# Performance work log

Hardware: AMD Instinct MI355X
Metric: run time of the kernel (lower is better)

The kernel has to match this reference:

```python
import jax, jax.numpy as jnp
import numpy as np

H = 5  # hidden size of both LSTMs

def _lstm_layer(x, Wih, Whh, bih, bhh):
    """x: [B,T,I] -> hs: [B,T,H]. PyTorch gate order i,f,g,o; zero init state."""
    B, T, _ = x.shape
    # precompute input contribution for all timesteps: [T,B,4H]
    xg = (jnp.einsum('bti,gi->btg', x, Wih) + bih + bhh).transpose(1, 0, 2)
    def step(carry, xg_t):
        h, c = carry
        g = xg_t + h @ Whh.T
        i, f, gg, o = jnp.split(g, 4, axis=-1)
        c = jax.nn.sigmoid(f) * c + jax.nn.sigmoid(i) * jnp.tanh(gg)
        h = jax.nn.sigmoid(o) * jnp.tanh(c)
        return (h, c), h
    h0 = jnp.zeros((B, H), x.dtype)
    (_, _), hs = jax.lax.scan(step, (h0, h0), xg)
    return hs.transpose(1, 0, 2)  # [B,T,H]

def setup_inputs() -> dict:
    key = jax.random.key(0)
    ks = jax.random.split(key, 32)
    B, T = 16384, 128
    def u(k, shape, fan):
        s = 1.0 / np.sqrt(fan)
        return jax.random.uniform(k, shape, jnp.float32, -s, s)
    inp = {
        'x1': jax.random.normal(ks[0], (B, T, 5), jnp.float32),
        'x2': jax.random.normal(ks[1], (B, T, 5), jnp.float32),
        # lstm1 (1 layer)
        'Wih1': u(ks[2], (4*H, 5), H), 'Whh1': u(ks[3], (4*H, H), H),
        'bih1': u(ks[4], (4*H,), H), 'bhh1': u(ks[5], (4*H,), H),
        # lstm2 layer 0
        'Wih2a': u(ks[6], (4*H, 5), H), 'Whh2a': u(ks[7], (4*H, H), H),
        'bih2a': u(ks[8], (4*H,), H), 'bhh2a': u(ks[9], (4*H,), H),
        # lstm2 layer 1
        'Wih2b': u(ks[10], (4*H, H), H), 'Whh2b': u(ks[11], (4*H, H), H),
        'bih2b': u(ks[12], (4*H,), H), 'bhh2b': u(ks[13], (4*H,), H),
        # FC stack 20->32->32->16->16->5
        'W1': u(ks[14], (32, 20), 20), 'b1': u(ks[15], (32,), 20),
        'W2': u(ks[16], (32, 32), 32), 'b2': u(ks[17], (32,), 32),
        'W3': u(ks[18], (16, 32), 32), 'b3': u(ks[19], (16,), 32),
        'W4': u(ks[20], (16, 16), 16), 'b4': u(ks[21], (16,), 16),
        'W5': u(ks[22], (5, 16), 16), 'b5': u(ks[23], (5,), 16),
    }
    return inp

def reference(x1, x2, Wih1, Whh1, bih1, bhh1, Wih2a, Whh2a, bih2a, bhh2a,
              Wih2b, Whh2b, bih2b, bhh2b, W1, b1, W2, b2, W3, b3, W4, b4, W5, b5):
    out1 = _lstm_layer(x1, Wih1, Whh1, bih1, bhh1)[:, -1, :]            # [B,5]
    h2 = _lstm_layer(x2, Wih2a, Whh2a, bih2a, bhh2a)                    # [B,T,5]
    out2 = _lstm_layer(h2, Wih2b, Whh2b, bih2b, bhh2b)[:, -1, :]        # [B,5]
    out = jnp.concatenate([x1[:, -1, :], x2[:, -1, :], out1, out2], axis=1)  # [B,20]
    out = jax.nn.relu(out @ W1.T + b1)
    out = jax.nn.relu(out @ W2.T + b2)
    out = jax.nn.relu(out @ W3.T + b3)
    out = jax.nn.relu(out @ W4.T + b4)
    return out @ W5.T + b5  # [B,5]
```

## Files before the change

kernel.cpp:

```cpp
#include <hip/hip_runtime.h>

#define DEV __device__ __forceinline__
#define KSIG (-1.442695041f)
#define KTANH (-2.885390082f)

typedef float f2 __attribute__((ext_vector_type(2)));

DEV float fexp2(float x) { return __builtin_amdgcn_exp2f(x); }
DEV float frcp(float x) { return __builtin_amdgcn_rcpf(x); }
DEV float bperm(int a, float x) {
  return __int_as_float(__builtin_amdgcn_ds_bpermute(a, __float_as_int(x)));
}
DEV f2 pkfma(f2 a, f2 b, f2 c) { return __builtin_elementwise_fma(a, b, c); }

struct CellP {
  f2 wx[4][2];
  f2 wh[4][2];
  float wx4[4], wh4[4];
  f2 b2[4];
};

DEV void load_cellP(CellP& W, int u, const float* __restrict__ Wih,
                    const float* __restrict__ Whh,
                    const float* __restrict__ bih,
                    const float* __restrict__ bhh) {
#pragma unroll
  for (int rt = 0; rt < 4; ++rt) {
    int row = 5 * rt + u;
    float kx = (rt == 2) ? KTANH : KSIG;
    W.wx[rt][0] = (f2){kx * Wih[row * 5 + 0], kx * Wih[row * 5 + 1]};
    W.wx[rt][1] = (f2){kx * Wih[row * 5 + 2], kx * Wih[row * 5 + 3]};
    W.wx4[rt] = kx * Wih[row * 5 + 4];
    W.wh[rt][0] = (f2){kx * Whh[row * 5 + 0], kx * Whh[row * 5 + 1]};
    W.wh[rt][1] = (f2){kx * Whh[row * 5 + 2], kx * Whh[row * 5 + 3]};
    W.wh4[rt] = kx * Whh[row * 5 + 4];
    W.b2[rt] = (f2){kx * (bih[row] + bhh[row]), 0.f};
  }
}

DEV float stepP(const CellP& W, const f2 xp[2], float x4, float hAll[5],
                float& c, const int bp[5]) {
  f2 hp0 = (f2){hAll[0], hAll[1]};
  f2 hp1 = (f2){hAll[2], hAll[3]};
  float acc[4];
#pragma unroll
  for (int rt = 0; rt < 4; ++rt) {
    f2 a2 = pkfma(W.wx[rt][0], xp[0], W.b2[rt]);
    a2 = pkfma(W.wx[rt][1], xp[1], a2);
    a2 = pkfma(W.wh[rt][0], hp0, a2);
    a2 = pkfma(W.wh[rt][1], hp1, a2);
    float a = a2.x + a2.y;
    a = fmaf(W.wx4[rt], x4, a);
    acc[rt] = fmaf(W.wh4[rt], hAll[4], a);
  }
  float gi = frcp(1.f + fexp2(acc[0]));
  float gf = frcp(1.f + fexp2(acc[1]));
  float gg = fmaf(2.f, frcp(1.f + fexp2(acc[2])), -1.f);
  float go = frcp(1.f + fexp2(acc[3]));
  c = fmaf(gf, c, gi * gg);
  float th = fmaf(2.f, frcp(1.f + fexp2(KTANH * c)), -1.f);
  float h = go * th;
#pragma unroll
  for (int u2 = 0; u2 < 5; ++u2) hAll[u2] = bperm(bp[u2], h);
  return h;
}

__global__ __launch_bounds__(192, 4) void rnn3w_kernel(
    const float* __restrict__ x1, const float* __restrict__ x2,
    const float* __restrict__ Wih1, const float* __restrict__ Whh1,
    const float* __restrict__ bih1, const float* __restrict__ bhh1,
    const float* __restrict__ Wih2a, const float* __restrict__ Whh2a,
    const float* __restrict__ bih2a, const float* __restrict__ bhh2a,
    const float* __restrict__ Wih2b, const float* __restrict__ Whh2b,
    const float* __restrict__ bih2b, const float* __restrict__ bhh2b,
    const float* __restrict__ W1, const float* __restrict__ b1,
    const float* __restrict__ W2, const float* __restrict__ b2,
    const float* __restrict__ W3, const float* __restrict__ b3,
    const float* __restrict__ W4, const float* __restrict__ b4,
    const float* __restrict__ W5, const float* __restrict__ b5,
    float* __restrict__ out, int B) {
  __shared__ float sH[2][64];
  __shared__ float sIn[12][20];
  __shared__ float sA[12][32];
  __shared__ float sB[12][32];

  const int tid = threadIdx.x;
  const int w = tid >> 6;
  const int l = tid & 63;
  const int g = l / 5;
  const int u = l - 5 * g;
  const bool act = (g < 12);
  const int el = act ? g : 11;
  const int eg = blockIdx.x * 12 + el;
  const int egc = (eg < B) ? eg : (B - 1);

  CellP W;
  if (w == 0)
    load_cellP(W, u, Wih1, Whh1, bih1, bhh1);
  else if (w == 1)
    load_cellP(W, u, Wih2a, Whh2a, bih2a, bhh2a);
  else
    load_cellP(W, u, Wih2b, Whh2b, bih2b, bhh2b);

  int bp[5];
#pragma unroll
  for (int u2 = 0; u2 < 5; ++u2) bp[u2] = (5 * g + u2) * 4;

  const float* px = ((w == 0) ? x1 : x2) + (size_t)egc * 640;

  if (tid < 128) sH[tid >> 6][tid & 63] = 0.f;

  float hAll[5];
  float c = 0.f, hOwn = 0.f;
#pragma unroll
  for (int k = 0; k < 5; ++k) hAll[k] = 0.f;

  f2 xp[2];
  float x4 = 0.f;
  if (w < 2) {
    xp[0] = (f2){px[0], px[1]};
    xp[1] = (f2){px[2], px[3]};
    x4 = px[4];
  }
  __syncthreads();

  for (int t = 0; t < 128; ++t) {
    f2 xin[2];
    float xin4;
    if (w == 2) {
      const float* s = &sH[(t + 1) & 1][g * 5];
      xin[0] = (f2){s[0], s[1]};
      xin[1] = (f2){s[2], s[3]};
      xin4 = s[4];
    } else {
      xin[0] = xp[0];
      xin[1] = xp[1];
      xin4 = x4;
    }
    if (w < 2) {
      const int tn = (t < 127) ? t + 1 : 127;
      xp[0] = (f2){px[tn * 5 + 0], px[tn * 5 + 1]};
      xp[1] = (f2){px[tn * 5 + 2], px[tn * 5 + 3]};
      x4 = px[tn * 5 + 4];
    }
    hOwn = stepP(W, xin, xin4, hAll, c, bp);
    if (w == 2 && t == 0) {
#pragma unroll
      for (int k = 0; k < 5; ++k) hAll[k] = 0.f;
      c = 0.f;
      hOwn = 0.f;
    }
    if (w == 1 && act) sH[t & 1][g * 5 + u] = hOwn;
    __syncthreads();
  }

  if (w == 2) {
    const float* s = &sH[1][g * 5];
    f2 xin[2] = {(f2){s[0], s[1]}, (f2){s[2], s[3]}};
    hOwn = stepP(W, xin, s[4], hAll, c, bp);
  }

  if (act) {
    if (w == 0) {
      sIn[el][u] = x1[(size_t)egc * 640 + 635 + u];
      sIn[el][10 + u] = hOwn;
    } else if (w == 1) {
      sIn[el][5 + u] = x2[(size_t)egc * 640 + 635 + u];
    } else {
      sIn[el][15 + u] = hOwn;
    }
  }
  __syncthreads();

  for (int task = tid; task < 12 * 32; task += 192) {
    int e = task >> 5, n = task & 31;
    float acc = b1[n];
#pragma unroll
    for (int k = 0; k < 20; ++k) acc = fmaf(W1[n * 20 + k], sIn[e][k], acc);
    sA[e][n] = fmaxf(acc, 0.f);
  }
  __syncthreads();
  for (int task = tid; task < 12 * 32; task += 192) {
    int e = task >> 5, n = task & 31;
    float acc = b2[n];
#pragma unroll
    for (int k = 0; k < 32; ++k) acc = fmaf(W2[n * 32 + k], sA[e][k], acc);
    sB[e][n] = fmaxf(acc, 0.f);
  }
  __syncthreads();
  {
    int e = tid >> 4, n = tid & 15;
    float acc = b3[n];
#pragma unroll
    for (int k = 0; k < 32; ++k) acc = fmaf(W3[n * 32 + k], sB[e][k], acc);
    sA[e][n] = fmaxf(acc, 0.f);
  }
  __syncthreads();
  {
    int e = tid >> 4, n = tid & 15;
    float acc = b4[n];
#pragma unroll
    for (int k = 0; k < 16; ++k) acc = fmaf(W4[n * 16 + k], sA[e][k], acc);
    sB[e][n] = fmaxf(acc, 0.f);
  }
  __syncthreads();
  if (tid < 60) {
    int e = tid / 5, n = tid - 5 * (tid / 5);
    float acc = b5[n];
#pragma unroll
    for (int k = 0; k < 16; ++k) acc = fmaf(W5[n * 16 + k], sB[e][k], acc);
    int ego = blockIdx.x * 12 + e;
    if (ego < B) out[(size_t)ego * 5 + n] = acc;
  }
}

extern "C" void kernel_launch(void* const* d_in, const int* in_sizes, int n_in,
                              void* d_out, int out_size, void* d_ws,
                              size_t ws_size, hipStream_t stream) {
  const float* x1 = (const float*)d_in[0];
  const float* x2 = (const float*)d_in[1];
  const float* Wih1 = (const float*)d_in[2];
  const float* Whh1 = (const float*)d_in[3];
  const float* bih1 = (const float*)d_in[4];
  const float* bhh1 = (const float*)d_in[5];
  const float* Wih2a = (const float*)d_in[6];
  const float* Whh2a = (const float*)d_in[7];
  const float* bih2a = (const float*)d_in[8];
  const float* bhh2a = (const float*)d_in[9];
  const float* Wih2b = (const float*)d_in[10];
  const float* Whh2b = (const float*)d_in[11];
  const float* bih2b = (const float*)d_in[12];
  const float* bhh2b = (const float*)d_in[13];
  const float* W1 = (const float*)d_in[14];
  const float* b1 = (const float*)d_in[15];
  const float* W2 = (const float*)d_in[16];
  const float* b2 = (const float*)d_in[17];
  const float* W3 = (const float*)d_in[18];
  const float* b3 = (const float*)d_in[19];
  const float* W4 = (const float*)d_in[20];
  const float* b4 = (const float*)d_in[21];
  const float* W5 = (const float*)d_in[22];
  const float* b5 = (const float*)d_in[23];

  int B = in_sizes[0] / 640;
  int nB = (B + 11) / 12;

  rnn3w_kernel<<<nB, 192, 0, stream>>>(
      x1, x2, Wih1, Whh1, bih1, bhh1, Wih2a, Whh2a, bih2a, bhh2a, Wih2b, Whh2b,
      bih2b, bhh2b, W1, b1, W2, b2, W3, b3, W4, b4, W5, b5, (float*)d_out, B);
}
```

Before: 223.5 us.

## Remove per-timestep block barriers by fusing stacked LSTM layers per wave

Instead of splitting the three LSTM layers across three waves joined by shared memory and a __syncthreads every timestep, each wave now runs independent sequences with no barriers. Wave 0 interleaves two lstm1 sequences, and waves 1 and 2 each run lstm2 layer0 and layer1 back to back within a single thread. Each block now handles 24 batch elements, and the FC stack loops are widened to match. The aim is to remove barrier stalls and give each wave two independent dependency chains for ILP, at the cost of more registers (launch bounds lowered to 2) and half as many blocks.

```diff
diff --git a/kernel.cpp b/kernel.cpp
--- a/kernel.cpp
+++ b/kernel.cpp
@@ -45,13 +45,13 @@
   float acc[4];
 #pragma unroll
   for (int rt = 0; rt < 4; ++rt) {
-    f2 a2 = pkfma(W.wx[rt][0], xp[0], W.b2[rt]);
+    f2 a2 = pkfma(W.wh[rt][0], hp0, W.b2[rt]);
+    a2 = pkfma(W.wh[rt][1], hp1, a2);
+    a2 = pkfma(W.wx[rt][0], xp[0], a2);
     a2 = pkfma(W.wx[rt][1], xp[1], a2);
-    a2 = pkfma(W.wh[rt][0], hp0, a2);
-    a2 = pkfma(W.wh[rt][1], hp1, a2);
     float a = a2.x + a2.y;
-    a = fmaf(W.wx4[rt], x4, a);
-    acc[rt] = fmaf(W.wh4[rt], hAll[4], a);
+    a = fmaf(W.wh4[rt], hAll[4], a);
+    acc[rt] = fmaf(W.wx4[rt], x4, a);
   }
   float gi = frcp(1.f + fexp2(acc[0]));
   float gf = frcp(1.f + fexp2(acc[1]));
@@ -65,7 +65,7 @@
   return h;
 }
 
-__global__ __launch_bounds__(192, 4) void rnn3w_kernel(
+__global__ __launch_bounds__(192, 2) void rnn_nosync_kernel(
     const float* __restrict__ x1, const float* __restrict__ x2,
     const float* __restrict__ Wih1, const float* __restrict__ Whh1,
     const float* __restrict__ bih1, const float* __restrict__ bhh1,
@@ -79,100 +79,96 @@
     const float* __restrict__ W4, const float* __restrict__ b4,
     const float* __restrict__ W5, const float* __restrict__ b5,
     float* __restrict__ out, int B) {
-  __shared__ float sH[2][64];
-  __shared__ float sIn[12][20];
-  __shared__ float sA[12][32];
-  __shared__ float sB[12][32];
+  __shared__ float sIn[24][20];
+  __shared__ float sA[24][32];
+  __shared__ float sB[24][32];
 
   const int tid = threadIdx.x;
   const int w = tid >> 6;
   const int l = tid & 63;
-  const int g = l / 5;
+  int g = l / 5;
   const int u = l - 5 * g;
   const bool act = (g < 12);
-  const int el = act ? g : 11;
-  const int eg = blockIdx.x * 12 + el;
-  const int egc = (eg < B) ? eg : (B - 1);
-
-  CellP W;
-  if (w == 0)
+  if (!act) g = 11;
+  const int base = blockIdx.x * 24;
+
+  int bp[5];
+#pragma unroll
+  for (int k = 0; k < 5; ++k) bp[k] = (5 * g + k) * 4;
+
+  if (w == 0) {
+    CellP W;
     load_cellP(W, u, Wih1, Whh1, bih1, bhh1);
-  else if (w == 1)
-    load_cellP(W, u, Wih2a, Whh2a, bih2a, bhh2a);
-  else
-    load_cellP(W, u, Wih2b, Whh2b, bih2b, bhh2b);
-
-  int bp[5];
-#pragma unroll
-  for (int u2 = 0; u2 < 5; ++u2) bp[u2] = (5 * g + u2) * 4;
-
-  const float* px = ((w == 0) ? x1 : x2) + (size_t)egc * 640;
-
-  if (tid < 128) sH[tid >> 6][tid & 63] = 0.f;
-
-  float hAll[5];
-  float c = 0.f, hOwn = 0.f;
-#pragma unroll
-  for (int k = 0; k < 5; ++k) hAll[k] = 0.f;
-
-  f2 xp[2];
-  float x4 = 0.f;
-  if (w < 2) {
-    xp[0] = (f2){px[0], px[1]};
-    xp[1] = (f2){px[2], px[3]};
-    x4 = px[4];
-  }
-  __syncthreads();
-
-  for (int t = 0; t < 128; ++t) {
-    f2 xin[2];
-    float xin4;
-    if (w == 2) {
-      const float* s = &sH[(t + 1) & 1][g * 5];
-      xin[0] = (f2){s[0], s[1]};
-      xin[1] = (f2){s[2], s[3]};
-      xin4 = s[4];
-    } else {
-      xin[0] = xp[0];
-      xin[1] = xp[1];
-      xin4 = x4;
-    }
-    if (w < 2) {
+    const int e0 = base + 2 * g, e1 = e0 + 1;
+    const int e0c = (e0 < B) ? e0 : B - 1;
+    const int e1c = (e1 < B) ? e1 : B - 1;
+    const float* p0 = x1 + (size_t)e0c * 640;
+    const float* p1 = x1 + (size_t)e1c * 640;
+    float hA[5], hB[5];
+    float cA = 0.f, cB = 0.f, hoA = 0.f, hoB = 0.f;
+#pragma unroll
+    for (int k = 0; k < 5; ++k) {
+      hA[k] = 0.f;
+      hB[k] = 0.f;
+    }
+    f2 xa[2] = {(f2){p0[0], p0[1]}, (f2){p0[2], p0[3]}};
+    f2 xb[2] = {(f2){p1[0], p1[1]}, (f2){p1[2], p1[3]}};
+    float xa4 = p0[4], xb4 = p1[4];
+    for (int t = 0; t < 128; ++t) {
+      f2 xia[2] = {xa[0], xa[1]}, xib[2] = {xb[0], xb[1]};
+      float xia4 = xa4, xib4 = xb4;
+      const int tn = (t < 127) ? t + 1 : 127;
+      xa[0] = (f2){p0[tn * 5 + 0], p0[tn * 5 + 1]};
+      xa[1] = (f2){p0[tn * 5 + 2], p0[tn * 5 + 3]};
+      xa4 = p0[tn * 5 + 4];
+      xb[0] = (f2){p1[tn * 5 + 0], p1[tn * 5 + 1]};
+      xb[1] = (f2){p1[tn * 5 + 2], p1[tn * 5 + 3]};
+      xb4 = p1[tn * 5 + 4];
+      hoA = stepP(W, xia, xia4, hA, cA, bp);
+      hoB = stepP(W, xib, xib4, hB, cB, bp);
+    }
+    if (act) {
+      sIn[2 * g][u] = x1[(size_t)e0c * 640 + 635 + u];
+      sIn[2 * g][10 + u] = hoA;
+      sIn[2 * g + 1][u] = x1[(size_t)e1c * 640 + 635 + u];
+      sIn[2 * g + 1][10 + u] = hoB;
+    }
+  } else {
+    CellP Wa, Wb;
+    load_cellP(Wa, u, Wih2a, Whh2a, bih2a, bhh2a);
+    load_cellP(Wb, u, Wih2b, Whh2b, bih2b, bhh2b);
+    const int el = ((w == 1) ? 0 : 12) + g;
+    const int e = base + el;
+    const int ec = (e < B) ? e : B - 1;
+    const float* px = x2 + (size_t)ec * 640;
+    float hA[5], hB[5];
+    float cA = 0.f, cB = 0.f, hoB = 0.f;
+#pragma unroll
+    for (int k = 0; k < 5; ++k) {
+      hA[k] = 0.f;
+      hB[k] = 0.f;
+    }
+    f2 xp[2] = {(f2){px[0], px[1]}, (f2){px[2], px[3]}};
+    float x4 = px[4];
+    for (int t = 0; t < 128; ++t) {
+      f2 xin[2] = {xp[0], xp[1]};
+      float xin4 = x4;
       const int tn = (t < 127) ? t + 1 : 127;
       xp[0] = (f2){px[tn * 5 + 0], px[tn * 5 + 1]};
       xp[1] = (f2){px[tn * 5 + 2], px[tn * 5 + 3]};
       x4 = px[tn * 5 + 4];
-    }
-    hOwn = stepP(W, xin, xin4, hAll, c, bp);
-    if (w == 2 && t == 0) {
-#pragma unroll
-      for (int k = 0; k < 5; ++k) hAll[k] = 0.f;
-      c = 0.f;
-      hOwn = 0.f;
-    }
-    if (w == 1 && act) sH[t & 1][g * 5 + u] = hOwn;
-    __syncthreads();
-  }
-
-  if (w == 2) {
-    const float* s = &sH[1][g * 5];
-    f2 xin[2] = {(f2){s[0], s[1]}, (f2){s[2], s[3]}};
-    hOwn = stepP(W, xin, s[4], hAll, c, bp);
-  }
-
-  if (act) {
-    if (w == 0) {
-      sIn[el][u] = x1[(size_t)egc * 640 + 635 + u];
-      sIn[el][10 + u] = hOwn;
-    } else if (w == 1) {
-      sIn[el][5 + u] = x2[(size_t)egc * 640 + 635 + u];
-    } else {
-      sIn[el][15 + u] = hOwn;
-    }
-  }
-  __syncthreads();
-
-  for (int task = tid; task < 12 * 32; task += 192) {
+      (void)stepP(Wa, xin, xin4, hA, cA, bp);
+      f2 hin[2] = {(f2){hA[0], hA[1]}, (f2){hA[2], hA[3]}};
+      hoB = stepP(Wb, hin, hA[4], hB, cB, bp);
+    }
+    if (act) {
+      sIn[el][5 + u] = x2[(size_t)ec * 640 + 635 + u];
+      sIn[el][15 + u] = hoB;
+    }
+  }
+  __syncthreads();
+
+  for (int task = tid; task < 24 * 32; task += 192) {
     int e = task >> 5, n = task & 31;
     float acc = b1[n];
 #pragma unroll
@@ -180,7 +176,7 @@
     sA[e][n] = fmaxf(acc, 0.f);
   }
   __syncthreads();
-  for (int task = tid; task < 12 * 32; task += 192) {
+  for (int task = tid; task < 24 * 32; task += 192) {
     int e = task >> 5, n = task & 31;
     float acc = b2[n];
 #pragma unroll
@@ -188,28 +184,28 @@
     sB[e][n] = fmaxf(acc, 0.f);
   }
   __syncthreads();
-  {
-    int e = tid >> 4, n = tid & 15;
+  for (int task = tid; task < 24 * 16; task += 192) {
+    int e = task >> 4, n = task & 15;
     float acc = b3[n];
 #pragma unroll
     for (int k = 0; k < 32; ++k) acc = fmaf(W3[n * 32 + k], sB[e][k], acc);
     sA[e][n] = fmaxf(acc, 0.f);
   }
   __syncthreads();
-  {
-    int e = tid >> 4, n = tid & 15;
+  for (int task = tid; task < 24 * 16; task += 192) {
+    int e = task >> 4, n = task & 15;
     float acc = b4[n];
 #pragma unroll
     for (int k = 0; k < 16; ++k) acc = fmaf(W4[n * 16 + k], sA[e][k], acc);
     sB[e][n] = fmaxf(acc, 0.f);
   }
   __syncthreads();
-  if (tid < 60) {
+  if (tid < 120) {
     int e = tid / 5, n = tid - 5 * (tid / 5);
     float acc = b5[n];
 #pragma unroll
     for (int k = 0; k < 16; ++k) acc = fmaf(W5[n * 16 + k], sB[e][k], acc);
-    int ego = blockIdx.x * 12 + e;
+    int ego = base + e;
     if (ego < B) out[(size_t)ego * 5 + n] = acc;
   }
 }
@@ -243,9 +239,9 @@
   const float* b5 = (const float*)d_in[23];
 
   int B = in_sizes[0] / 640;
-  int nB = (B + 11) / 12;
-
-  rnn3w_kernel<<<nB, 192, 0, stream>>>(
+  int nB = (B + 23) / 24;
+
+  rnn_nosync_kernel<<<nB, 192, 0, stream>>>(
       x1, x2, Wih1, Whh1, bih1, bhh1, Wih2a, Whh2a, bih2a, bhh2a, Wih2b, Whh2b,
       bih2b, bhh2b, W1, b1, W2, b2, W3, b3, W4, b4, W5, b5, (float*)d_out, B);
 }
```

Result: slower. 239.0 us (+6.9%).

## Map one batch element per lane with full LSTM cell held in registers

Applied to the files above, without the earlier changes.

Replaces the five-lanes-per-element layout, which exchanged hidden state through ds_bpermute, with one element per lane. Each lane computes all 20 gates with packed FMAs over weights held in registers. Inputs are loaded as 80-byte float4 chunks, double-buffered, and the time loop is unrolled by chunk with a bare s_barrier sync. Blocks now cover 64 elements, so there are far fewer blocks. In exchange, register pressure rises sharply (about 100 weight registers, hence launch_bounds(192,1)), and each lane's input reads are strided by 2560 bytes across lanes, so loads no longer coalesce.

```diff
diff --git a/kernel.cpp b/kernel.cpp
--- a/kernel.cpp
+++ b/kernel.cpp
@@ -5,67 +5,141 @@
 #define KTANH (-2.885390082f)
 
 typedef float f2 __attribute__((ext_vector_type(2)));
+typedef float f4 __attribute__((ext_vector_type(4)));
 
 DEV float fexp2(float x) { return __builtin_amdgcn_exp2f(x); }
 DEV float frcp(float x) { return __builtin_amdgcn_rcpf(x); }
-DEV float bperm(int a, float x) {
-  return __int_as_float(__builtin_amdgcn_ds_bpermute(a, __float_as_int(x)));
-}
 DEV f2 pkfma(f2 a, f2 b, f2 c) { return __builtin_elementwise_fma(a, b, c); }
 
-struct CellP {
-  f2 wx[4][2];
-  f2 wh[4][2];
-  float wx4[4], wh4[4];
-  f2 b2[4];
+DEV void pin2(f2& v) {
+  float a = v.x, b = v.y;
+  asm volatile("" : "+v"(a), "+v"(b));
+  v = (f2){a, b};
+}
+
+DEV void sync_lds() {
+  asm volatile("s_waitcnt lgkmcnt(0)\ns_barrier" ::: "memory");
+}
+
+struct CellU {
+  f2 wx[2][5][5];
+  f2 wh[2][5][5];
+  f2 bb[2][5];
 };
 
-DEV void load_cellP(CellP& W, int u, const float* __restrict__ Wih,
+DEV void load_cellU(CellU& W, const float* __restrict__ Wih,
                     const float* __restrict__ Whh,
                     const float* __restrict__ bih,
                     const float* __restrict__ bhh) {
 #pragma unroll
-  for (int rt = 0; rt < 4; ++rt) {
-    int row = 5 * rt + u;
-    float kx = (rt == 2) ? KTANH : KSIG;
-    W.wx[rt][0] = (f2){kx * Wih[row * 5 + 0], kx * Wih[row * 5 + 1]};
-    W.wx[rt][1] = (f2){kx * Wih[row * 5 + 2], kx * Wih[row * 5 + 3]};
-    W.wx4[rt] = kx * Wih[row * 5 + 4];
-    W.wh[rt][0] = (f2){kx * Whh[row * 5 + 0], kx * Whh[row * 5 + 1]};
-    W.wh[rt][1] = (f2){kx * Whh[row * 5 + 2], kx * Whh[row * 5 + 3]};
-    W.wh4[rt] = kx * Whh[row * 5 + 4];
-    W.b2[rt] = (f2){kx * (bih[row] + bhh[row]), 0.f};
-  }
-}
-
-DEV float stepP(const CellP& W, const f2 xp[2], float x4, float hAll[5],
-                float& c, const int bp[5]) {
-  f2 hp0 = (f2){hAll[0], hAll[1]};
-  f2 hp1 = (f2){hAll[2], hAll[3]};
-  float acc[4];
-#pragma unroll
-  for (int rt = 0; rt < 4; ++rt) {
-    f2 a2 = pkfma(W.wx[rt][0], xp[0], W.b2[rt]);
-    a2 = pkfma(W.wx[rt][1], xp[1], a2);
-    a2 = pkfma(W.wh[rt][0], hp0, a2);
-    a2 = pkfma(W.wh[rt][1], hp1, a2);
-    float a = a2.x + a2.y;
-    a = fmaf(W.wx4[rt], x4, a);
-    acc[rt] = fmaf(W.wh4[rt], hAll[4], a);
-  }
-  float gi = frcp(1.f + fexp2(acc[0]));
-  float gf = frcp(1.f + fexp2(acc[1]));
-  float gg = fmaf(2.f, frcp(1.f + fexp2(acc[2])), -1.f);
-  float go = frcp(1.f + fexp2(acc[3]));
-  c = fmaf(gf, c, gi * gg);
-  float th = fmaf(2.f, frcp(1.f + fexp2(KTANH * c)), -1.f);
-  float h = go * th;
-#pragma unroll
-  for (int u2 = 0; u2 < 5; ++u2) hAll[u2] = bperm(bp[u2], h);
-  return h;
-}
-
-__global__ __launch_bounds__(192, 4) void rnn3w_kernel(
+  for (int j = 0; j < 5; ++j) {
+#pragma unroll
+    for (int k = 0; k < 5; ++k) {
+      W.wx[0][j][k] = (f2){KSIG * Wih[j * 5 + k], KSIG * Wih[(5 + j) * 5 + k]};
+      W.wx[1][j][k] =
+          (f2){KTANH * Wih[(10 + j) * 5 + k], KSIG * Wih[(15 + j) * 5 + k]};
+      W.wh[0][j][k] = (f2){KSIG * Whh[j * 5 + k], KSIG * Whh[(5 + j) * 5 + k]};
+      W.wh[1][j][k] =
+          (f2){KTANH * Whh[(10 + j) * 5 + k], KSIG * Whh[(15 + j) * 5 + k]};
+    }
+    W.bb[0][j] =
+        (f2){KSIG * (bih[j] + bhh[j]), KSIG * (bih[5 + j] + bhh[5 + j])};
+    W.bb[1][j] = (f2){KTANH * (bih[10 + j] + bhh[10 + j]),
+                      KSIG * (bih[15 + j] + bhh[15 + j])};
+  }
+}
+
+DEV void stepU(const CellU& W, float x0, float x1, float x2, float x3, float x4,
+               float h[5], float c[5]) {
+  f2 aIF[5], aGO[5];
+#pragma unroll
+  for (int j = 0; j < 5; ++j) {
+    aIF[j] = W.bb[0][j];
+    aGO[j] = W.bb[1][j];
+  }
+  float xs[5] = {x0, x1, x2, x3, x4};
+#pragma unroll
+  for (int k = 0; k < 5; ++k) {
+    f2 xk = (f2){xs[k], xs[k]};
+#pragma unroll
+    for (int j = 0; j < 5; ++j) {
+      aIF[j] = pkfma(W.wx[0][j][k], xk, aIF[j]);
+      aGO[j] = pkfma(W.wx[1][j][k], xk, aGO[j]);
+    }
+  }
+#pragma unroll
+  for (int k = 0; k < 5; ++k) {
+    f2 hk = (f2){h[k], h[k]};
+#pragma unroll
+    for (int j = 0; j < 5; ++j) {
+      aIF[j] = pkfma(W.wh[0][j][k], hk, aIF[j]);
+      aGO[j] = pkfma(W.wh[1][j][k], hk, aGO[j]);
+    }
+  }
+#pragma unroll
+  for (int j = 0; j < 5; ++j) {
+    float gi = frcp(1.f + fexp2(aIF[j].x));
+    float gf = frcp(1.f + fexp2(aIF[j].y));
+    float tg = fmaf(2.f, frcp(1.f + fexp2(aGO[j].x)), -1.f);
+    float go = frcp(1.f + fexp2(aGO[j].y));
+    c[j] = fmaf(gf, c[j], gi * tg);
+    float tc = fmaf(2.f, frcp(1.f + fexp2(KTANH * c[j])), -1.f);
+    h[j] = go * tc;
+  }
+}
+
+struct XBuf {
+  f4 a, b, c, d, e;
+};
+DEV void xload(XBuf& bf, const float* __restrict__ px, int ch) {
+  const f4* q = (const f4*)px + ch * 5;
+  bf.a = q[0];
+  bf.b = q[1];
+  bf.c = q[2];
+  bf.d = q[3];
+  bf.e = q[4];
+}
+
+#define STEP_S(S, RST, X0, X1, X2, X3, X4)                 \
+  {                                                        \
+    float xv0, xv1, xv2, xv3, xv4;                         \
+    if (w == 2) {                                          \
+      const int rb = ((S) + 1) & 1;                        \
+      xv0 = sH[rb][l][0];                                  \
+      xv1 = sH[rb][l][1];                                  \
+      xv2 = sH[rb][l][2];                                  \
+      xv3 = sH[rb][l][3];                                  \
+      xv4 = sH[rb][l][4];                                  \
+    } else {                                               \
+      xv0 = X0;                                            \
+      xv1 = X1;                                            \
+      xv2 = X2;                                            \
+      xv3 = X3;                                            \
+      xv4 = X4;                                            \
+    }                                                      \
+    stepU(W, xv0, xv1, xv2, xv3, xv4, h, c);               \
+    if (w == 1) {                                          \
+      const int wb = (S) & 1;                              \
+      sH[wb][l][0] = h[0];                                 \
+      sH[wb][l][1] = h[1];                                 \
+      sH[wb][l][2] = h[2];                                 \
+      sH[wb][l][3] = h[3];                                 \
+      sH[wb][l][4] = h[4];                                 \
+    }                                                      \
+    if ((RST) && w == 2) {  \
+      h[0] = h[1] = h[2] = h[3] = h[4] = 0.f;              \
+      c[0] = c[1] = c[2] = c[3] = c[4] = 0.f;              \
+    }                                                      \
+    sync_lds();                                            \
+  }
+
+#define CHUNK(X, RST)                                 \
+  STEP_S(0, RST, X.a.x, X.a.y, X.a.z, X.a.w, X.b.x)   \
+  STEP_S(1, false, X.b.y, X.b.z, X.b.w, X.c.x, X.c.y) \
+  STEP_S(2, false, X.c.z, X.c.w, X.d.x, X.d.y, X.d.z) \
+  STEP_S(3, false, X.d.w, X.e.x, X.e.y, X.e.z, X.e.w)
+
+__global__ __launch_bounds__(192, 1) void rnn_epl_kernel(
     const float* __restrict__ x1, const float* __restrict__ x2,
     const float* __restrict__ Wih1, const float* __restrict__ Whh1,
     const float* __restrict__ bih1, const float* __restrict__ bhh1,
@@ -79,137 +153,117 @@
     const float* __restrict__ W4, const float* __restrict__ b4,
     const float* __restrict__ W5, const float* __restrict__ b5,
     float* __restrict__ out, int B) {
-  __shared__ float sH[2][64];
-  __shared__ float sIn[12][20];
-  __shared__ float sA[12][32];
-  __shared__ float sB[12][32];
+  __shared__ float sH[2][64][5];
+  __shared__ float sIn[64][20];
+  __shared__ float sA[64][32];
+  __shared__ float sB[64][32];
 
   const int tid = threadIdx.x;
   const int w = tid >> 6;
   const int l = tid & 63;
-  const int g = l / 5;
-  const int u = l - 5 * g;
-  const bool act = (g < 12);
-  const int el = act ? g : 11;
-  const int eg = blockIdx.x * 12 + el;
-  const int egc = (eg < B) ? eg : (B - 1);
-
-  CellP W;
+  const int e = blockIdx.x * 64 + l;
+  const int ec = (e < B) ? e : (B - 1);
+
+  CellU W;
   if (w == 0)
-    load_cellP(W, u, Wih1, Whh1, bih1, bhh1);
+    load_cellU(W, Wih1, Whh1, bih1, bhh1);
   else if (w == 1)
-    load_cellP(W, u, Wih2a, Whh2a, bih2a, bhh2a);
+    load_cellU(W, Wih2a, Whh2a, bih2a, bhh2a);
   else
-    load_cellP(W, u, Wih2b, Whh2b, bih2b, bhh2b);
-
-  int bp[5];
-#pragma unroll
-  for (int u2 = 0; u2 < 5; ++u2) bp[u2] = (5 * g + u2) * 4;
-
-  const float* px = ((w == 0) ? x1 : x2) + (size_t)egc * 640;
-
-  if (tid < 128) sH[tid >> 6][tid & 63] = 0.f;
-
-  float hAll[5];
-  float c = 0.f, hOwn = 0.f;
-#pragma unroll
-  for (int k = 0; k < 5; ++k) hAll[k] = 0.f;
-
-  f2 xp[2];
-  float x4 = 0.f;
-  if (w < 2) {
-    xp[0] = (f2){px[0], px[1]};
-    xp[1] = (f2){px[2], px[3]};
-    x4 = px[4];
-  }
-  __syncthreads();
-
-  for (int t = 0; t < 128; ++t) {
-    f2 xin[2];
-    float xin4;
-    if (w == 2) {
-      const float* s = &sH[(t + 1) & 1][g * 5];
-      xin[0] = (f2){s[0], s[1]};
-      xin[1] = (f2){s[2], s[3]};
-      xin4 = s[4];
-    } else {
-      xin[0] = xp[0];
-      xin[1] = xp[1];
-      xin4 = x4;
+    load_cellU(W, Wih2b, Whh2b, bih2b, bhh2b);
+#pragma unroll
+  for (int p = 0; p < 2; ++p) {
+#pragma unroll
+    for (int j = 0; j < 5; ++j) {
+#pragma unroll
+      for (int k = 0; k < 5; ++k) {
+        pin2(W.wx[p][j][k]);
+        pin2(W.wh[p][j][k]);
+      }
+      pin2(W.bb[p][j]);
     }
-    if (w < 2) {
-      const int tn = (t < 127) ? t + 1 : 127;
-      xp[0] = (f2){px[tn * 5 + 0], px[tn * 5 + 1]};
-      xp[1] = (f2){px[tn * 5 + 2], px[tn * 5 + 3]};
-      x4 = px[tn * 5 + 4];
-    }
-    hOwn = stepP(W, xin, xin4, hAll, c, bp);
-    if (w == 2 && t == 0) {
-#pragma unroll
-      for (int k = 0; k < 5; ++k) hAll[k] = 0.f;
-      c = 0.f;
-      hOwn = 0.f;
-    }
-    if (w == 1 && act) sH[t & 1][g * 5 + u] = hOwn;
-    __syncthreads();
+  }
+
+  const float* px = ((w == 0) ? x1 : x2) + (size_t)ec * 640;
+
+  for (int i = tid; i < 2 * 64 * 5; i += 192) ((float*)sH)[i] = 0.f;
+
+  float h[5], c[5];
+#pragma unroll
+  for (int j = 0; j < 5; ++j) {
+    h[j] = 0.f;
+    c[j] = 0.f;
+  }
+
+  XBuf cur{}, nxt{};
+  if (w < 2) xload(cur, px, 0);
+  __syncthreads();
+
+  for (int ch = 0; ch < 32; ch += 2) {
+    if (w < 2) xload(nxt, px, ch + 1);
+    const bool rst = (ch == 0);
+    CHUNK(cur, rst);
+    if (w < 2) xload(cur, px, (ch + 2 < 32) ? ch + 2 : 31);
+    CHUNK(nxt, false);
   }
 
   if (w == 2) {
-    const float* s = &sH[1][g * 5];
-    f2 xin[2] = {(f2){s[0], s[1]}, (f2){s[2], s[3]}};
-    hOwn = stepP(W, xin, s[4], hAll, c, bp);
-  }
-
-  if (act) {
-    if (w == 0) {
-      sIn[el][u] = x1[(size_t)egc * 640 + 635 + u];
-      sIn[el][10 + u] = hOwn;
-    } else if (w == 1) {
-      sIn[el][5 + u] = x2[(size_t)egc * 640 + 635 + u];
-    } else {
-      sIn[el][15 + u] = hOwn;
-    }
-  }
-  __syncthreads();
-
-  for (int task = tid; task < 12 * 32; task += 192) {
-    int e = task >> 5, n = task & 31;
+    stepU(W, sH[1][l][0], sH[1][l][1], sH[1][l][2], sH[1][l][3], sH[1][l][4],
+          h, c);
+  }
+
+  if (w == 0) {
+#pragma unroll
+    for (int k = 0; k < 5; ++k) sIn[l][k] = px[635 + k];
+#pragma unroll
+    for (int j = 0; j < 5; ++j) sIn[l][10 + j] = h[j];
+  } else if (w == 1) {
+#pragma unroll
+    for (int k = 0; k < 5; ++k) sIn[l][5 + k] = px[635 + k];
+  } else {
+#pragma unroll
+    for (int j = 0; j < 5; ++j) sIn[l][15 + j] = h[j];
+  }
+  __syncthreads();
+
+  for (int task = tid; task < 64 * 32; task += 192) {
+    int e2 = task >> 5, n = task & 31;
     float acc = b1[n];
 #pragma unroll
-    for (int k = 0; k < 20; ++k) acc = fmaf(W1[n * 20 + k], sIn[e][k], acc);
-    sA[e][n] = fmaxf(acc, 0.f);
-  }
-  __syncthreads();
-  for (int task = tid; task < 12 * 32; task += 192) {
-    int e = task >> 5, n = task & 31;
+    for (int k = 0; k < 20; ++k) acc = fmaf(W1[n * 20 + k], sIn[e2][k], acc);
+    sA[e2][n] = fmaxf(acc, 0.f);
+  }
+  __syncthreads();
+  for (int task = tid; task < 64 * 32; task += 192) {
+    int e2 = task >> 5, n = task & 31;
     float acc = b2[n];
 #pragma unroll
-    for (int k = 0; k < 32; ++k) acc = fmaf(W2[n * 32 + k], sA[e][k], acc);
-    sB[e][n] = fmaxf(acc, 0.f);
-  }
-  __syncthreads();
-  {
-    int e = tid >> 4, n = tid & 15;
+    for (int k = 0; k < 32; ++k) acc = fmaf(W2[n * 32 + k], sA[e2][k], acc);
+    sB[e2][n] = fmaxf(acc, 0.f);
+  }
+  __syncthreads();
+  for (int task = tid; task < 64 * 16; task += 192) {
+    int e2 = task >> 4, n = task & 15;
     float acc = b3[n];
 #pragma unroll
-    for (int k = 0; k < 32; ++k) acc = fmaf(W3[n * 32 + k], sB[e][k], acc);
-    sA[e][n] = fmaxf(acc, 0.f);
-  }
-  __syncthreads();
-  {
-    int e = tid >> 4, n = tid & 15;
+    for (int k = 0; k < 32; ++k) acc = fmaf(W3[n * 32 + k], sB[e2][k], acc);
+    sA[e2][n] = fmaxf(acc, 0.f);
+  }
+  __syncthreads();
+  for (int task = tid; task < 64 * 16; task += 192) {
+    int e2 = task >> 4, n = task & 15;
     float acc = b4[n];
 #pragma unroll
-    for (int k = 0; k < 16; ++k) acc = fmaf(W4[n * 16 + k], sA[e][k], acc);
-    sB[e][n] = fmaxf(acc, 0.f);
-  }
-  __syncthreads();
-  if (tid < 60) {
-    int e = tid / 5, n = tid - 5 * (tid / 5);
+    for (int k = 0; k < 16; ++k) acc = fmaf(W4[n * 16 + k], sA[e2][k], acc);
+    sB[e2][n] = fmaxf(acc, 0.f);
+  }
+  __syncthreads();
+  for (int task = tid; task < 64 * 5; task += 192) {
+    int e2 = task / 5, n = task - 5 * (task / 5);
     float acc = b5[n];
 #pragma unroll
-    for (int k = 0; k < 16; ++k) acc = fmaf(W5[n * 16 + k], sB[e][k], acc);
-    int ego = blockIdx.x * 12 + e;
+    for (int k = 0; k < 16; ++k) acc = fmaf(W5[n * 16 + k], sB[e2][k], acc);
+    int ego = blockIdx.x * 64 + e2;
     if (ego < B) out[(size_t)ego * 5 + n] = acc;
   }
 }
@@ -243,9 +297,9 @@
   const float* b5 = (const float*)d_in[23];
 
   int B = in_sizes[0] / 640;
-  int nB = (B + 11) / 12;
-
-  rnn3w_kernel<<<nB, 192, 0, stream>>>(
+  int nB = (B + 63) / 64;
+
+  rnn_epl_kernel<<<nB, 192, 0, stream>>>(
       x1, x2, Wih1, Whh1, bih1, bhh1, Wih2a, Whh2a, bih2a, bhh2a, Wih2b, Whh2b,
       bih2b, bhh2b, W1, b1, W2, b2, W3, b3, W4, b4, W5, b5, (float*)d_out, B);
 }
```

Measured after the change: 231.7 us. +3.7%, slower.

## Vectorize x loads into 4-step chunks with double buffering and lighter barriers

Applied to the files above, without the earlier changes.

Input timesteps are now loaded as five float4 vectors covering four timesteps, double-buffered one chunk ahead, instead of five scalar loads per step. The step loop is unrolled per chunk, packed-FMA gate math is replaced with scalar FMA chains, and __syncthreads is swapped for an inline s_waitcnt lgkmcnt + s_barrier. The goal is fewer global load instructions and more latency hiding across the serial recurrence. In exchange it uses more registers, and launch bounds drop from 4 to 2 blocks per SM, which may reduce occupancy. The inline barrier waits only on LDS, so global memory ordering relies on the data being register-only.

```diff
diff --git a/kernel.cpp b/kernel.cpp
--- a/kernel.cpp
+++ b/kernel.cpp
@@ -4,23 +4,25 @@
 #define KSIG (-1.442695041f)
 #define KTANH (-2.885390082f)
 
-typedef float f2 __attribute__((ext_vector_type(2)));
+typedef float f4 __attribute__((ext_vector_type(4)));
 
 DEV float fexp2(float x) { return __builtin_amdgcn_exp2f(x); }
 DEV float frcp(float x) { return __builtin_amdgcn_rcpf(x); }
 DEV float bperm(int a, float x) {
   return __int_as_float(__builtin_amdgcn_ds_bpermute(a, __float_as_int(x)));
 }
-DEV f2 pkfma(f2 a, f2 b, f2 c) { return __builtin_elementwise_fma(a, b, c); }
-
-struct CellP {
-  f2 wx[4][2];
-  f2 wh[4][2];
-  float wx4[4], wh4[4];
-  f2 b2[4];
+
+DEV void sync_lds() {
+  asm volatile("s_waitcnt lgkmcnt(0)\ns_barrier" ::: "memory");
+}
+
+struct CellS {
+  float wx[4][5];
+  float wh[4][5];
+  float b[4];
 };
 
-DEV void load_cellP(CellP& W, int u, const float* __restrict__ Wih,
+DEV void load_cellS(CellS& W, int u, const float* __restrict__ Wih,
                     const float* __restrict__ Whh,
                     const float* __restrict__ bih,
                     const float* __restrict__ bhh) {
@@ -28,30 +30,31 @@
   for (int rt = 0; rt < 4; ++rt) {
     int row = 5 * rt + u;
     float kx = (rt == 2) ? KTANH : KSIG;
-    W.wx[rt][0] = (f2){kx * Wih[row * 5 + 0], kx * Wih[row * 5 + 1]};
-    W.wx[rt][1] = (f2){kx * Wih[row * 5 + 2], kx * Wih[row * 5 + 3]};
-    W.wx4[rt] = kx * Wih[row * 5 + 4];
-    W.wh[rt][0] = (f2){kx * Whh[row * 5 + 0], kx * Whh[row * 5 + 1]};
-    W.wh[rt][1] = (f2){kx * Whh[row * 5 + 2], kx * Whh[row * 5 + 3]};
-    W.wh4[rt] = kx * Whh[row * 5 + 4];
-    W.b2[rt] = (f2){kx * (bih[row] + bhh[row]), 0.f};
-  }
-}
-
-DEV float stepP(const CellP& W, const f2 xp[2], float x4, float hAll[5],
-                float& c, const int bp[5]) {
-  f2 hp0 = (f2){hAll[0], hAll[1]};
-  f2 hp1 = (f2){hAll[2], hAll[3]};
+#pragma unroll
+    for (int k = 0; k < 5; ++k) {
+      W.wx[rt][k] = kx * Wih[row * 5 + k];
+      W.wh[rt][k] = kx * Whh[row * 5 + k];
+    }
+    W.b[rt] = kx * (bih[row] + bhh[row]);
+  }
+}
+
+DEV float stepS(const CellS& W, float x0, float x1, float x2, float x3,
+                float x4, float hAll[5], float& c, const int bp[5]) {
   float acc[4];
 #pragma unroll
   for (int rt = 0; rt < 4; ++rt) {
-    f2 a2 = pkfma(W.wx[rt][0], xp[0], W.b2[rt]);
-    a2 = pkfma(W.wx[rt][1], xp[1], a2);
-    a2 = pkfma(W.wh[rt][0], hp0, a2);
-    a2 = pkfma(W.wh[rt][1], hp1, a2);
-    float a = a2.x + a2.y;
-    a = fmaf(W.wx4[rt], x4, a);
-    acc[rt] = fmaf(W.wh4[rt], hAll[4], a);
+    float a = W.b[rt];
+    a = fmaf(W.wx[rt][0], x0, a);
+    a = fmaf(W.wx[rt][1], x1, a);
+    a = fmaf(W.wx[rt][2], x2, a);
+    a = fmaf(W.wx[rt][3], x3, a);
+    a = fmaf(W.wx[rt][4], x4, a);
+    a = fmaf(W.wh[rt][0], hAll[0], a);
+    a = fmaf(W.wh[rt][1], hAll[1], a);
+    a = fmaf(W.wh[rt][2], hAll[2], a);
+    a = fmaf(W.wh[rt][3], hAll[3], a);
+    acc[rt] = fmaf(W.wh[rt][4], hAll[4], a);
   }
   float gi = frcp(1.f + fexp2(acc[0]));
   float gf = frcp(1.f + fexp2(acc[1]));
@@ -65,7 +68,52 @@
   return h;
 }
 
-__global__ __launch_bounds__(192, 4) void rnn3w_kernel(
+struct XBuf {
+  f4 a, b, c, d, e;
+};
+DEV void xload(XBuf& bf, const float* __restrict__ px, int ch) {
+  const f4* q = (const f4*)px + ch * 5;
+  bf.a = q[0];
+  bf.b = q[1];
+  bf.c = q[2];
+  bf.d = q[3];
+  bf.e = q[4];
+}
+
+#define STEP_S(S, RST, X0, X1, X2, X3, X4)                    \
+  {                                                           \
+    float xv0, xv1, xv2, xv3, xv4;                            \
+    if (w == 2) {                                             \
+      const float* s = &sH[((S) + 1) & 1][g * 5];             \
+      xv0 = s[0];                                             \
+      xv1 = s[1];                                             \
+      xv2 = s[2];                                             \
+      xv3 = s[3];                                             \
+      xv4 = s[4];                                             \
+    } else {                                                  \
+      xv0 = X0;                                               \
+      xv1 = X1;                                               \
+      xv2 = X2;                                               \
+      xv3 = X3;                                               \
+      xv4 = X4;                                               \
+    }                                                         \
+    hOwn = stepS(W, xv0, xv1, xv2, xv3, xv4, hAll, c, bp);    \
+    if (w == 1 && act) sH[(S) & 1][g * 5 + u] = hOwn;         \
+    if ((RST) && w == 2) {                                    \
+      hAll[0] = hAll[1] = hAll[2] = hAll[3] = hAll[4] = 0.f;  \
+      c = 0.f;                                                \
+      hOwn = 0.f;                                             \
+    }                                                         \
+    sync_lds();                                               \
+  }
+
+#define CHUNK(X, RST)                                 \
+  STEP_S(0, RST, X.a.x, X.a.y, X.a.z, X.a.w, X.b.x)   \
+  STEP_S(1, false, X.b.y, X.b.z, X.b.w, X.c.x, X.c.y) \
+  STEP_S(2, false, X.c.z, X.c.w, X.d.x, X.d.y, X.d.z) \
+  STEP_S(3, false, X.d.w, X.e.x, X.e.y, X.e.z, X.e.w)
+
+__global__ __launch_bounds__(192, 2) void rnn_s_kernel(
     const float* __restrict__ x1, const float* __restrict__ x2,
     const float* __restrict__ Wih1, const float* __restrict__ Whh1,
     const float* __restrict__ bih1, const float* __restrict__ bhh1,
@@ -87,24 +135,24 @@
   const int tid = threadIdx.x;
   const int w = tid >> 6;
   const int l = tid & 63;
-  const int g = l / 5;
+  int g = l / 5;
   const int u = l - 5 * g;
   const bool act = (g < 12);
-  const int el = act ? g : 11;
-  const int eg = blockIdx.x * 12 + el;
+  if (!act) g = 11;
+  const int eg = blockIdx.x * 12 + g;
   const int egc = (eg < B) ? eg : (B - 1);
 
-  CellP W;
+  CellS W;
   if (w == 0)
-    load_cellP(W, u, Wih1, Whh1, bih1, bhh1);
+    load_cellS(W, u, Wih1, Whh1, bih1, bhh1);
   else if (w == 1)
-    load_cellP(W, u, Wih2a, Whh2a, bih2a, bhh2a);
+    load_cellS(W, u, Wih2a, Whh2a, bih2a, bhh2a);
   else
-    load_cellP(W, u, Wih2b, Whh2b, bih2b, bhh2b);
+    load_cellS(W, u, Wih2b, Whh2b, bih2b, bhh2b);
 
   int bp[5];
 #pragma unroll
-  for (int u2 = 0; u2 < 5; ++u2) bp[u2] = (5 * g + u2) * 4;
+  for (int k = 0; k < 5; ++k) bp[k] = (5 * g + k) * 4;
 
   const float* px = ((w == 0) ? x1 : x2) + (size_t)egc * 640;
 
@@ -115,59 +163,31 @@
 #pragma unroll
   for (int k = 0; k < 5; ++k) hAll[k] = 0.f;
 
-  f2 xp[2];
-  float x4 = 0.f;
-  if (w < 2) {
-    xp[0] = (f2){px[0], px[1]};
-    xp[1] = (f2){px[2], px[3]};
-    x4 = px[4];
-  }
-  __syncthreads();
-
-  for (int t = 0; t < 128; ++t) {
-    f2 xin[2];
-    float xin4;
-    if (w == 2) {
-      const float* s = &sH[(t + 1) & 1][g * 5];
-      xin[0] = (f2){s[0], s[1]};
-      xin[1] = (f2){s[2], s[3]};
-      xin4 = s[4];
-    } else {
-      xin[0] = xp[0];
-      xin[1] = xp[1];
-      xin4 = x4;
-    }
-    if (w < 2) {
-      const int tn = (t < 127) ? t + 1 : 127;
-      xp[0] = (f2){px[tn * 5 + 0], px[tn * 5 + 1]};
-      xp[1] = (f2){px[tn * 5 + 2], px[tn * 5 + 3]};
-      x4 = px[tn * 5 + 4];
-    }
-    hOwn = stepP(W, xin, xin4, hAll, c, bp);
-    if (w == 2 && t == 0) {
-#pragma unroll
-      for (int k = 0; k < 5; ++k) hAll[k] = 0.f;
-      c = 0.f;
-      hOwn = 0.f;
-    }
-    if (w == 1 && act) sH[t & 1][g * 5 + u] = hOwn;
-    __syncthreads();
+  XBuf cur{}, nxt{};
+  if (w < 2) xload(cur, px, 0);
+  __syncthreads();
+
+  for (int ch = 0; ch < 32; ch += 2) {
+    if (w < 2) xload(nxt, px, (ch + 1 < 32) ? ch + 1 : 31);
+    const bool rst = (ch == 0);
+    CHUNK(cur, rst);
+    if (w < 2) xload(cur, px, (ch + 2 < 32) ? ch + 2 : 31);
+    CHUNK(nxt, false);
   }
 
   if (w == 2) {
     const float* s = &sH[1][g * 5];
-    f2 xin[2] = {(f2){s[0], s[1]}, (f2){s[2], s[3]}};
-    hOwn = stepP(W, xin, s[4], hAll, c, bp);
+    hOwn = stepS(W, s[0], s[1], s[2], s[3], s[4], hAll, c, bp);
   }
 
   if (act) {
     if (w == 0) {
-      sIn[el][u] = x1[(size_t)egc * 640 + 635 + u];
-      sIn[el][10 + u] = hOwn;
+      sIn[g][u] = x1[(size_t)egc * 640 + 635 + u];
+      sIn[g][10 + u] = hOwn;
     } else if (w == 1) {
-      sIn[el][5 + u] = x2[(size_t)egc * 640 + 635 + u];
+      sIn[g][5 + u] = x2[(size_t)egc * 640 + 635 + u];
     } else {
-      sIn[el][15 + u] = hOwn;
+      sIn[g][15 + u] = hOwn;
     }
   }
   __syncthreads();
@@ -245,7 +265,7 @@
   int B = in_sizes[0] / 640;
   int nB = (B + 11) / 12;
 
-  rnn3w_kernel<<<nB, 192, 0, stream>>>(
+  rnn_s_kernel<<<nB, 192, 0, stream>>>(
       x1, x2, Wih1, Whh1, bih1, bhh1, Wih2a, Whh2a, bih2a, bhh2a, Wih2b, Whh2b,
       bih2b, bhh2b, W1, b1, W2, b2, W3, b3, W4, b4, W5, b5, (float*)d_out, B);
 }
```

New measurement: 239.6 us. 1.07x slower.
